# Kernel tuning notes

Measured on AMD Instinct MI355X. Metric: run time of the kernel, lower is better.

Reference implementation:

```python
import jax, jax.numpy as jnp
import numpy as np

MARGIN = 0.1


def setup_inputs() -> dict:
    key = jax.random.key(0)
    k1, k2 = jax.random.split(key)
    N, G = 262144, 128
    inputs = jax.random.normal(k1, (N, G), dtype=jnp.float32)
    labels = jax.random.randint(k2, (N,), 0, G, dtype=jnp.int64)
    return {"inputs": inputs, "labels": labels}


def reference(inputs, labels):
    # inputs: [N, G] scores, labels: [N] correct gloss index.
    # MarginRankingLoss(x1=correct, x2=other, y=1):
    #   mean over N*(G-1) pairs of max(0, margin - (correct - other))
    N, G = inputs.shape
    correct = jnp.take_along_axis(inputs, labels[:, None], axis=1)  # [N, 1]
    hinge = jnp.maximum(MARGIN - correct + inputs, 0.0)             # [N, G]
    mask = jnp.arange(G)[None, :] != labels[:, None]                # exclude j == label
    total = jnp.sum(jnp.where(mask, hinge, 0.0))
    return total / (N * (G - 1))
```

## Files before the change

### kernel.cpp

```cpp
#include <hip/hip_runtime.h>

#define MARGIN 0.1f

__global__ __launch_bounds__(256) void margin_loss_kernel(
    const float* __restrict__ inputs,
    const int*   __restrict__ labels,
    float*       __restrict__ out,
    int N, float inv_denom)
{
    const int G = 128;
    const int tid     = blockIdx.x * blockDim.x + threadIdx.x;
    const int group   = tid >> 5;
    const int lane32  = tid & 31;
    const int ngroups = (gridDim.x * blockDim.x) >> 5;

    float partial = 0.0f;

    for (int row = group; row < N; row += ngroups) {
        const int lbl = labels[row];
        const float4 v = ((const float4*)(inputs + (size_t)row * G))[lane32];

        float cand;
        switch (lbl & 3) {
            case 0:  cand = v.x; break;
            case 1:  cand = v.y; break;
            case 2:  cand = v.z; break;
            default: cand = v.w; break;
        }
        const float correct = __shfl(cand, lbl >> 2, 32);

        float s = fmaxf(MARGIN - correct + v.x, 0.0f)
                + fmaxf(MARGIN - correct + v.y, 0.0f)
                + fmaxf(MARGIN - correct + v.z, 0.0f)
                + fmaxf(MARGIN - correct + v.w, 0.0f);

        if (lane32 == 0) s -= MARGIN;

        partial += s;
    }

    #pragma unroll
    for (int off = 32; off > 0; off >>= 1)
        partial += __shfl_down(partial, off, 64);

    __shared__ float wsum[4];
    const int wave = threadIdx.x >> 6;
    if ((threadIdx.x & 63) == 0) wsum[wave] = partial;
    __syncthreads();

    if (threadIdx.x == 0) {
        const float bs = (wsum[0] + wsum[1]) + (wsum[2] + wsum[3]);
        atomicAdd(out, bs * inv_denom);
    }
}

extern "C" void kernel_launch(void* const* d_in, const int* in_sizes, int n_in,
                              void* d_out, int out_size, void* d_ws, size_t ws_size,
                              hipStream_t stream) {
    const float* inputs = (const float*)d_in[0];
    const int*   labels = (const int*)d_in[1];
    float*       out    = (float*)d_out;

    const int N = in_sizes[1];
    const int G = 128;
    const float inv_denom = 1.0f / ((float)N * (float)(G - 1));

    hipMemsetAsync(out, 0, sizeof(float), stream);

    const int block = 256;
    const int grid  = 2048;
    margin_loss_kernel<<<grid, block, 0, stream>>>(inputs, labels, out, N, inv_denom);
}
```

Measured before the change: 205.3 us.

## Batch four rows per load with vector labels and two-pass reduction

Each 32-lane group now handles 16 consecutive rows, loading four rows' float4s and a four-label int4 before computing, which raises memory-level parallelism per thread. The per-row margin correction for the label column is applied once at the end as MARGIN*N. The memset and float atomic are replaced by per-block partials written to workspace and summed by a single-block finalize kernel, which adds a second launch. The code assumes N is a multiple of 16 and 16-byte-aligned labels, and that labels are 32-bit although the task declares int64.

```diff
diff --git a/kernel.cpp b/kernel.cpp
--- a/kernel.cpp
+++ b/kernel.cpp
@@ -1,14 +1,17 @@
 #include <hip/hip_runtime.h>
 
 #define MARGIN 0.1f
+#define NBLOCKS 2048
+#define BLOCK 256
 
-__global__ __launch_bounds__(256) void margin_loss_kernel(
+__global__ __launch_bounds__(BLOCK) void margin_partials_kernel(
     const float* __restrict__ inputs,
     const int*   __restrict__ labels,
-    float*       __restrict__ out,
-    int N, float inv_denom)
+    float*       __restrict__ partials,
+    int N)
 {
     const int G = 128;
+    const int ROWS_PER_GROUP = 16;
     const int tid     = blockIdx.x * blockDim.x + threadIdx.x;
     const int group   = tid >> 5;
     const int lane32  = tid & 31;
@@ -16,41 +19,79 @@
 
     float partial = 0.0f;
 
-    for (int row = group; row < N; row += ngroups) {
-        const int lbl = labels[row];
-        const float4 v = ((const float4*)(inputs + (size_t)row * G))[lane32];
+    for (int base = group * ROWS_PER_GROUP; base < N;
+         base += ngroups * ROWS_PER_GROUP) {
+        #pragma unroll
+        for (int c = 0; c < ROWS_PER_GROUP; c += 4) {
+            const int r0 = base + c;
+            const int4 lab = *(const int4*)(labels + r0);
 
-        float cand;
-        switch (lbl & 3) {
-            case 0:  cand = v.x; break;
-            case 1:  cand = v.y; break;
-            case 2:  cand = v.z; break;
-            default: cand = v.w; break;
+            const float4 v0 = ((const float4*)(inputs + (size_t)(r0 + 0) * G))[lane32];
+            const float4 v1 = ((const float4*)(inputs + (size_t)(r0 + 1) * G))[lane32];
+            const float4 v2 = ((const float4*)(inputs + (size_t)(r0 + 2) * G))[lane32];
+            const float4 v3 = ((const float4*)(inputs + (size_t)(r0 + 3) * G))[lane32];
+
+            #pragma unroll
+            for (int k = 0; k < 4; ++k) {
+                const int lbl = (k == 0) ? lab.x : (k == 1) ? lab.y
+                              : (k == 2) ? lab.z : lab.w;
+                const float4 v = (k == 0) ? v0 : (k == 1) ? v1
+                               : (k == 2) ? v2 : v3;
+                float cand;
+                switch (lbl & 3) {
+                    case 0:  cand = v.x; break;
+                    case 1:  cand = v.y; break;
+                    case 2:  cand = v.z; break;
+                    default: cand = v.w; break;
+                }
+                const float mc = MARGIN - __shfl(cand, lbl >> 2, 32);
+                partial += fmaxf(mc + v.x, 0.0f) + fmaxf(mc + v.y, 0.0f)
+                         + fmaxf(mc + v.z, 0.0f) + fmaxf(mc + v.w, 0.0f);
+            }
         }
-        const float correct = __shfl(cand, lbl >> 2, 32);
-
-        float s = fmaxf(MARGIN - correct + v.x, 0.0f)
-                + fmaxf(MARGIN - correct + v.y, 0.0f)
-                + fmaxf(MARGIN - correct + v.z, 0.0f)
-                + fmaxf(MARGIN - correct + v.w, 0.0f);
-
-        if (lane32 == 0) s -= MARGIN;
-
-        partial += s;
     }
 
     #pragma unroll
     for (int off = 32; off > 0; off >>= 1)
         partial += __shfl_down(partial, off, 64);
 
-    __shared__ float wsum[4];
+    __shared__ float wsum[BLOCK / 64];
     const int wave = threadIdx.x >> 6;
     if ((threadIdx.x & 63) == 0) wsum[wave] = partial;
     __syncthreads();
 
     if (threadIdx.x == 0) {
-        const float bs = (wsum[0] + wsum[1]) + (wsum[2] + wsum[3]);
-        atomicAdd(out, bs * inv_denom);
+        float bs = 0.0f;
+        #pragma unroll
+        for (int w = 0; w < BLOCK / 64; ++w) bs += wsum[w];
+        partials[blockIdx.x] = bs;
+    }
+}
+
+__global__ __launch_bounds__(BLOCK) void margin_finalize_kernel(
+    const float* __restrict__ partials,
+    float*       __restrict__ out,
+    int N, float inv_denom)
+{
+    float s = 0.0f;
+    for (int i = threadIdx.x; i < NBLOCKS; i += BLOCK)
+        s += partials[i];
+
+    #pragma unroll
+    for (int off = 32; off > 0; off >>= 1)
+        s += __shfl_down(s, off, 64);
+
+    __shared__ float wsum[BLOCK / 64];
+    const int wave = threadIdx.x >> 6;
+    if ((threadIdx.x & 63) == 0) wsum[wave] = s;
+    __syncthreads();
+
+    if (threadIdx.x == 0) {
+        float total = 0.0f;
+        #pragma unroll
+        for (int w = 0; w < BLOCK / 64; ++w) total += wsum[w];
+        total -= MARGIN * (float)N;
+        *out = total * inv_denom;
     }
 }
 
@@ -60,14 +101,12 @@
     const float* inputs = (const float*)d_in[0];
     const int*   labels = (const int*)d_in[1];
     float*       out    = (float*)d_out;
+    float*       partials = (float*)d_ws;
 
     const int N = in_sizes[1];
     const int G = 128;
     const float inv_denom = 1.0f / ((float)N * (float)(G - 1));
 
-    hipMemsetAsync(out, 0, sizeof(float), stream);
-
-    const int block = 256;
-    const int grid  = 2048;
-    margin_loss_kernel<<<grid, block, 0, stream>>>(inputs, labels, out, N, inv_denom);
+    margin_partials_kernel<<<NBLOCKS, BLOCK, 0, stream>>>(inputs, labels, partials, N);
+    margin_finalize_kernel<<<1, BLOCK, 0, stream>>>(partials, out, N, inv_denom);
 }
```

Result: faster. 191.9 us (-6.6%).
